# Kernel optimization log

Hardware: AMD Instinct MI355X
Metric: run time of the kernel (lower is better)

## Reference

```python
import jax, jax.numpy as jnp
import numpy as np

FS = 4096.0
TRAIN_KERNEL = 4
TRAIN_STRIDE = 0.25
BATCH = 1024
NPERSEG = 4096          # fftlength * fs
NOVERLAP = NPERSEG // 2 # default overlap
FL, FH = 20.0, 500.0


def _welch(data):
    """Faithful port of _torch_welch with average='mean' (which is a SUM over segments
    in the original code), off by the same constant factor as the original."""
    N, nsample = data.shape
    nstride = NPERSEG - NOVERLAP
    nseg = int(np.ceil((nsample - NPERSEG) / nstride)) + 1
    # frame indices [nseg, nperseg] (static numpy -> cheap gather)
    idx = np.arange(nseg)[:, None] * nstride + np.arange(NPERSEG)[None, :]
    frames = data[:, idx]                                   # [N, nseg, nperseg]
    n = np.arange(NPERSEG)
    window = (0.5 - 0.5 * np.cos(2.0 * np.pi * n / NPERSEG)).astype(np.float32) * 2.0  # periodic hann * 2
    fd = jnp.fft.rfft(frames * window, axis=-1)             # [N, nseg, nfreq]
    power = jnp.real(fd) ** 2 + jnp.imag(fd) ** 2
    psd = jnp.sum(power, axis=1)                            # original 'mean' branch uses sum
    T = nsample * FS
    return psd / T                                          # [N, nfreq]


def setup_inputs() -> dict:
    key = jax.random.key(0)
    k1, k2 = jax.random.split(key)
    T = int(TRAIN_KERNEL * FS)  # 16384
    pred = jax.random.normal(k1, (BATCH, T), dtype=jnp.float32)
    target = jax.random.normal(k2, (BATCH, T), dtype=jnp.float32)
    return {"pred": pred, "target": target}


def reference(pred, target):
    res = target - pred
    s = int(TRAIN_STRIDE * FS)                     # 1024 samples per stride
    shape_x = int(TRAIN_KERNEL / TRAIN_STRIDE)     # 16
    # cross[i] = res[:, i*s:(i+1)*s].flatten() -> reshape/transpose, no loop
    def to_cross(x):
        return x[:, : shape_x * s].reshape(BATCH, shape_x, s).transpose(1, 0, 2).reshape(shape_x, BATCH * s)
    cross_res = to_cross(res)
    cross_target = to_cross(target)

    psd_res = _welch(cross_res)                    # [shape_x, nfreq]
    psd_target = _welch(cross_target)

    nfreq = NPERSEG // 2 + 1
    freq = np.linspace(0.0, FS / 2.0, nfreq)
    mask = jnp.asarray((FL < freq) & (freq < FH))
    dfreq = float(freq[1] - freq[0])
    scale = FH - FL

    psd_res = jnp.where(mask, psd_res, 0.0)
    psd_ratio = psd_res / psd_target
    loss = jnp.sum(psd_ratio, axis=1) * dfreq / scale  # [shape_x]
    return jnp.mean(loss[-8:]) * loss.shape[0]
```

## Files before the change

kernel.cpp:

```cpp
#include <hip/hip_runtime.h>

#define NSEG 511
#define NROWS 8
#define ROW0 8
#define K0 21
#define KEND 500
#define NFREQ 479
#define ACC_STRIDE 512
#define ACC_ELEMS (2 * NROWS * ACC_STRIDE)
#define NREP 8
#define SPB 4
#define NGROUPS 128
#define NBLOCKS (2 * NROWS * NGROUPS)

__device__ __forceinline__ int sw(int i) { return i ^ (((i >> 5) & 7) << 2); }
__device__ __forceinline__ int ms(int m) { return m ^ ((m >> 6) & 7); }

__device__ __forceinline__ float2 cmul(float2 a, float2 b) {
    return make_float2(fmaf(a.x, b.x, -a.y * b.y), fmaf(a.x, b.y, a.y * b.x));
}
__device__ __forceinline__ float2 cadd(float2 a, float2 b) { return make_float2(a.x + b.x, a.y + b.y); }
__device__ __forceinline__ float2 csub(float2 a, float2 b) { return make_float2(a.x - b.x, a.y - b.y); }

__device__ __forceinline__ void dft8(float2& x0, float2& x1, float2& x2, float2& x3,
                                     float2& x4, float2& x5, float2& x6, float2& x7) {
    const float C45 = 0.70710678118654752440f;
    float2 t0 = cadd(x0, x4), u0 = csub(x0, x4);
    float2 t1 = cadd(x1, x5), u1 = csub(x1, x5);
    float2 t2 = cadd(x2, x6), u2 = csub(x2, x6);
    float2 t3 = cadd(x3, x7), u3 = csub(x3, x7);
    float2 s0 = cadd(t0, t2), d0 = csub(t0, t2);
    float2 s1 = cadd(t1, t3), d1 = csub(t1, t3);
    float2 v1 = make_float2(C45 * (u1.x + u1.y), C45 * (u1.y - u1.x));
    float2 v2 = make_float2(u2.y, -u2.x);
    float2 v3 = make_float2(C45 * (u3.y - u3.x), -C45 * (u3.x + u3.y));
    float2 s2 = cadd(u0, v2), d2 = csub(u0, v2);
    float2 s3 = cadd(v1, v3), d3 = csub(v1, v3);
    float2 mid1 = make_float2(d1.y, -d1.x);
    float2 mid3 = make_float2(d3.y, -d3.x);
    x0 = cadd(s0, s1); x4 = csub(s0, s1);
    x2 = cadd(d0, mid1); x6 = csub(d0, mid1);
    x1 = cadd(s2, s3); x5 = csub(s2, s3);
    x3 = cadd(d2, mid3); x7 = csub(d2, mid3);
}

__device__ __forceinline__ void twiddle8cs(float2& x1, float2& x2, float2& x3, float2& x4,
                                           float2& x5, float2& x6, float2& x7,
                                           float c, float s) {
    float2 w1 = make_float2(c, s);
    float2 w2 = cmul(w1, w1);
    float2 w3 = cmul(w2, w1);
    float2 w4 = cmul(w2, w2);
    float2 w5 = cmul(w4, w1);
    float2 w6 = cmul(w3, w3);
    float2 w7 = cmul(w4, w3);
    x1 = cmul(x1, w1); x2 = cmul(x2, w2); x3 = cmul(x3, w3);
    x4 = cmul(x4, w4); x5 = cmul(x5, w5); x6 = cmul(x6, w6);
    x7 = cmul(x7, w7);
}

__global__ __launch_bounds__(256)
void psd_kernel(const float* __restrict__ pred,
                const float* __restrict__ target,
                float* __restrict__ acc) {
    __shared__ float2 buf[2048];
    __shared__ float2 nat[1024];

    const int bid = blockIdx.x;
    const int grp = bid % NGROUPS;
    const int row = (bid / NGROUPS) % NROWS + ROW0;
    const int sig = bid / (NGROUPS * NROWS);
    const int tid = threadIdx.x;
    const int seg0 = grp * SPB;
    const int ns = (seg0 + SPB <= NSEG) ? SPB : (NSEG - seg0);
    float* accR = acc + (bid & (NREP - 1)) * ACC_ELEMS;

    const float2* t2p = (const float2*)target;
    const float2* p2p = (const float2*)pred;

    const int base = 2 * seg0 * 8192 + row * 512 + tid;
#define LOADRAW(X, IDX)                                                      \
    {                                                                        \
        int _i = (IDX);                                                      \
        float2 v = t2p[_i];                                                  \
        if (sig == 0) { float2 p = p2p[_i]; v.x -= p.x; v.y -= p.y; }        \
        X = v;                                                               \
    }
    float2 r0, r1, r2, r3, r4, r5, r6, r7;
    LOADRAW(r0, base)
    LOADRAW(r1, base + 256)
    LOADRAW(r2, base + 8192)
    LOADRAW(r3, base + 8448)
    LOADRAW(r4, base + 16384)
    LOADRAW(r5, base + 16640)
    LOADRAW(r6, base + 24576)
    LOADRAW(r7, base + 24832)

    const float WA = 3.06796157577128245e-3f;
    const float CD = 0.99999882344642529f;
    const float SD = 1.53398018628476550e-3f;
    const float H  = 0.70710678118654752440f;
    float sa, ca;
    __sincosf((float)tid * WA, &sa, &ca);
    float2 wv0, wv1, wv2, wv3, wv4, wv5, wv6, wv7;
#define MKW(W, CE, SE) { float cr = (CE), sr = (SE);                         \
        W = make_float2(1.0f - cr, 1.0f - (cr * CD - sr * SD)); }
    MKW(wv0, ca, sa)
    MKW(wv1, H * (ca - sa), H * (sa + ca))
    MKW(wv2, -sa, ca)
    MKW(wv3, -H * (ca + sa), H * (ca - sa))
    MKW(wv4, -ca, -sa)
    MKW(wv5, H * (sa - ca), -H * (sa + ca))
    MKW(wv6, sa, -ca)
    MKW(wv7, H * (ca + sa), H * (sa - ca))
#undef MKW
    float sb, cb;
    __sincosf((float)(tid & 31) * -2.45436926061702596e-2f, &sb, &cb);
    float cc, ss;
    {
        const float TC1 = 0.98078528040323044913f, TS1 = -0.19509032201612826785f;
        const float TC2 = 0.92387953251128675613f, TS2 = -0.38268343236508977173f;
        const float TC3 = 0.83146961230254523708f, TS3 = -0.55557023301960222474f;
        int mq = tid & 3;
        cc = (mq & 2) ? ((mq & 1) ? TC3 : TC2) : ((mq & 1) ? TC1 : 1.0f);
        ss = (mq & 2) ? ((mq & 1) ? TS3 : TS2) : ((mq & 1) ? TS1 : 0.0f);
    }
    float sn0, cs0, sn1, cs1;
    __sincosf(-1.53398078788564123e-3f * (float)(K0 + tid), &sn0, &cs0);
    {
        const float CU = 0.98078528040323044913f;
        const float SU = 0.19509032201612826785f;
        cs1 = cs0 * CU + sn0 * SU;
        sn1 = sn0 * CU - cs0 * SU;
    }

    float pw1 = 0.0f, pw2 = 0.0f;
    float4* b4 = (float4*)buf;

    #pragma unroll 1
    for (int s = 0; s < ns; ++s) {
        float2 x0 = make_float2(r0.x * wv0.x, r0.y * wv0.y);
        float2 x1 = make_float2(r1.x * wv1.x, r1.y * wv1.y);
        float2 x2 = make_float2(r2.x * wv2.x, r2.y * wv2.y);
        float2 x3 = make_float2(r3.x * wv3.x, r3.y * wv3.y);
        float2 x4 = make_float2(r4.x * wv4.x, r4.y * wv4.y);
        float2 x5 = make_float2(r5.x * wv5.x, r5.y * wv5.y);
        float2 x6 = make_float2(r6.x * wv6.x, r6.y * wv6.y);
        float2 x7 = make_float2(r7.x * wv7.x, r7.y * wv7.y);

        if (s + 1 < ns) {
            r0 = r4; r1 = r5; r2 = r6; r3 = r7;
            int nb = base + (s + 1) * 16384;
            LOADRAW(r4, nb + 16384)
            LOADRAW(r5, nb + 16640)
            LOADRAW(r6, nb + 24576)
            LOADRAW(r7, nb + 24832)
        }

        dft8(x0, x1, x2, x3, x4, x5, x6, x7);
        twiddle8cs(x1, x2, x3, x4, x5, x6, x7, ca, -sa);
        buf[sw(tid)]        = x0;
        buf[sw(tid + 256)]  = x1;
        buf[sw(tid + 512)]  = x2;
        buf[sw(tid + 768)]  = x3;
        buf[sw(tid + 1024)] = x4;
        buf[sw(tid + 1280)] = x5;
        buf[sw(tid + 1536)] = x6;
        buf[sw(tid + 1792)] = x7;
        __syncthreads();

        {
            const int baseB = (tid & 31) + 256 * (tid >> 5);
            x0 = buf[sw(baseB)];
            x1 = buf[sw(baseB + 32)];
            x2 = buf[sw(baseB + 64)];
            x3 = buf[sw(baseB + 96)];
            x4 = buf[sw(baseB + 128)];
            x5 = buf[sw(baseB + 160)];
            x6 = buf[sw(baseB + 192)];
            x7 = buf[sw(baseB + 224)];
            dft8(x0, x1, x2, x3, x4, x5, x6, x7);
            twiddle8cs(x1, x2, x3, x4, x5, x6, x7, cb, sb);
            buf[sw(baseB)]       = x0;
            buf[sw(baseB + 32)]  = x1;
            buf[sw(baseB + 64)]  = x2;
            buf[sw(baseB + 96)]  = x3;
            buf[sw(baseB + 128)] = x4;
            buf[sw(baseB + 160)] = x5;
            buf[sw(baseB + 192)] = x6;
            buf[sw(baseB + 224)] = x7;
        }
        __syncthreads();

        {
            const int baseC = (tid & 3) + 32 * ((tid >> 2) & 7) + 256 * (tid >> 5);
            x0 = buf[sw(baseC)];
            x1 = buf[sw(baseC + 4)];
            x2 = buf[sw(baseC + 8)];
            x3 = buf[sw(baseC + 12)];
            x4 = buf[sw(baseC + 16)];
            x5 = buf[sw(baseC + 20)];
            x6 = buf[sw(baseC + 24)];
            x7 = buf[sw(baseC + 28)];
            dft8(x0, x1, x2, x3, x4, x5, x6, x7);
            twiddle8cs(x1, x2, x3, x4, x5, x6, x7, cc, ss);
            buf[sw(baseC)]      = x0;
            buf[sw(baseC + 4)]  = x1;
            buf[sw(baseC + 8)]  = x2;
            buf[sw(baseC + 12)] = x3;
            buf[sw(baseC + 16)] = x4;
            buf[sw(baseC + 20)] = x5;
            buf[sw(baseC + 24)] = x6;
            buf[sw(baseC + 28)] = x7;
        }
        __syncthreads();

#define QUAD(N)                                                              \
        {                                                                    \
            int n = (N);                                                     \
            int q4 = sw(4 * n) >> 1;                                         \
            float4 lo = b4[q4], hi = b4[q4 + 1];                             \
            float2 X0 = make_float2((lo.x + hi.x) + (lo.z + hi.z),           \
                                    (lo.y + hi.y) + (lo.w + hi.w));          \
            float D0x = lo.x - hi.x, D0y = lo.y - hi.y;                      \
            float D1x = lo.z - hi.z, D1y = lo.w - hi.w;                      \
            float2 X3 = make_float2(D0x - D1y, D0y + D1x);                   \
            int m = 64 * (n & 7) + 8 * ((n >> 3) & 7) + (n >> 6);            \
            int a = ms(m);                                                   \
            nat[a] = X0;                                                     \
            nat[512 + a] = X3;                                               \
        }
        QUAD(tid)
        QUAD(tid + 256)
#undef QUAD
        __syncthreads();

        {
            int k = K0 + tid;
            float2 zk = nat[ms(k)];
            float2 zn = nat[512 + ms(512 - k)];
            float Ex = 0.5f * (zk.x + zn.x);
            float Ey = 0.5f * (zk.y - zn.y);
            float Ox = 0.5f * (zk.y + zn.y);
            float Oy = -0.5f * (zk.x - zn.x);
            float xr = Ex + Ox * cs0 - Oy * sn0;
            float xi = Ey + Ox * sn0 + Oy * cs0;
            pw1 += xr * xr + xi * xi;
        }
        if (tid < KEND - K0 - 256) {
            int k = K0 + 256 + tid;
            float2 zk = nat[ms(k)];
            float2 zn = nat[512 + ms(512 - k)];
            float Ex = 0.5f * (zk.x + zn.x);
            float Ey = 0.5f * (zk.y - zn.y);
            float Ox = 0.5f * (zk.y + zn.y);
            float Oy = -0.5f * (zk.x - zn.x);
            float xr = Ex + Ox * cs1 - Oy * sn1;
            float xi = Ey + Ox * sn1 + Oy * cs1;
            pw2 += xr * xr + xi * xi;
        }
        __syncthreads();
    }

    {
        int i0 = (sig * NROWS + (row - ROW0)) * ACC_STRIDE;
        atomicAdd(&accR[i0 + tid], pw1);
        if (tid < KEND - K0 - 256) atomicAdd(&accR[i0 + 256 + tid], pw2);
    }
#undef LOADRAW
}

__global__ __launch_bounds__(256)
void reduce_kernel(const float* __restrict__ acc, float* __restrict__ out) {
    __shared__ float sh[256];
    int tid = threadIdx.x;
    float sum = 0.0f;
    for (int n = tid; n < NROWS * NFREQ; n += 256) {
        int r = n / NFREQ, k = n % NFREQ;
        float num = 0.0f, den = 0.0f;
        #pragma unroll
        for (int rep = 0; rep < NREP; ++rep) {
            num += acc[rep * ACC_ELEMS + r * ACC_STRIDE + k];
            den += acc[rep * ACC_ELEMS + (NROWS + r) * ACC_STRIDE + k];
        }
        sum += num / den;
    }
    sh[tid] = sum;
    __syncthreads();
    for (int s = 128; s > 0; s >>= 1) {
        if (tid < s) sh[tid] += sh[tid + s];
        __syncthreads();
    }
    if (tid == 0) out[0] = sh[0] * (1.0f / 240.0f);
}

extern "C" void kernel_launch(void* const* d_in, const int* in_sizes, int n_in,
                              void* d_out, int out_size, void* d_ws, size_t ws_size,
                              hipStream_t stream) {
    const float* pred = (const float*)d_in[0];
    const float* target = (const float*)d_in[1];
    float* acc = (float*)d_ws;

    hipMemsetAsync(acc, 0, NREP * ACC_ELEMS * sizeof(float), stream);
    psd_kernel<<<NBLOCKS, 256, 0, stream>>>(pred, target, acc);
    reduce_kernel<<<1, 256, 0, stream>>>(acc, (float*)d_out);
}
```

Measured before the change: 170.2 us.

## Fuse final radix-4 stage into the power epilogue and drop syncs

The intermediate `nat` shared buffer and its scatter pass are removed. Each thread now reads the needed quads straight from `buf` using precomputed bit-reversed indices and does the final radix-4 butterfly inline during the PSD accumulation. This cuts a full LDS write/read round trip and two barriers per segment. The trailing barrier is now skipped on the last iteration. The barrier between the second and third FFT stages is dropped, which relies on each stage's data staying within one wavefront. Window coefficients are recomputed each iteration behind an asm barrier to cut register pressure, and launch bounds request 6 blocks per CU, trading extra ALU work for occupancy.

```diff
diff --git a/kernel.cpp b/kernel.cpp
--- a/kernel.cpp
+++ b/kernel.cpp
@@ -14,7 +14,7 @@
 #define NBLOCKS (2 * NROWS * NGROUPS)
 
 __device__ __forceinline__ int sw(int i) { return i ^ (((i >> 5) & 7) << 2); }
-__device__ __forceinline__ int ms(int m) { return m ^ ((m >> 6) & 7); }
+__device__ __forceinline__ int revq(int m) { return 64 * (m & 7) + 8 * ((m >> 3) & 7) + (m >> 6); }
 
 __device__ __forceinline__ float2 cmul(float2 a, float2 b) {
     return make_float2(fmaf(a.x, b.x, -a.y * b.y), fmaf(a.x, b.y, a.y * b.x));
@@ -59,12 +59,11 @@
     x7 = cmul(x7, w7);
 }
 
-__global__ __launch_bounds__(256)
+__global__ __launch_bounds__(256, 6)
 void psd_kernel(const float* __restrict__ pred,
                 const float* __restrict__ target,
                 float* __restrict__ acc) {
     __shared__ float2 buf[2048];
-    __shared__ float2 nat[1024];
 
     const int bid = blockIdx.x;
     const int grp = bid % NGROUPS;
@@ -102,18 +101,6 @@
     const float H  = 0.70710678118654752440f;
     float sa, ca;
     __sincosf((float)tid * WA, &sa, &ca);
-    float2 wv0, wv1, wv2, wv3, wv4, wv5, wv6, wv7;
-#define MKW(W, CE, SE) { float cr = (CE), sr = (SE);                         \
-        W = make_float2(1.0f - cr, 1.0f - (cr * CD - sr * SD)); }
-    MKW(wv0, ca, sa)
-    MKW(wv1, H * (ca - sa), H * (sa + ca))
-    MKW(wv2, -sa, ca)
-    MKW(wv3, -H * (ca + sa), H * (ca - sa))
-    MKW(wv4, -ca, -sa)
-    MKW(wv5, H * (sa - ca), -H * (sa + ca))
-    MKW(wv6, sa, -ca)
-    MKW(wv7, H * (ca + sa), H * (sa - ca))
-#undef MKW
     float sb, cb;
     __sincosf((float)(tid & 31) * -2.45436926061702596e-2f, &sb, &cb);
     float cc, ss;
@@ -133,12 +120,34 @@
         cs1 = cs0 * CU + sn0 * SU;
         sn1 = sn0 * CU - cs0 * SU;
     }
+    const int qA1 = sw(4 * revq(K0 + tid)) >> 1;
+    const int qB1 = sw(4 * revq(512 - (K0 + tid))) >> 1;
+    int qA2 = 0, qB2 = 0;
+    if (tid < KEND - K0 - 256) {
+        qA2 = sw(4 * revq(K0 + 256 + tid)) >> 1;
+        qB2 = sw(4 * revq(512 - (K0 + 256 + tid))) >> 1;
+    }
 
     float pw1 = 0.0f, pw2 = 0.0f;
     float4* b4 = (float4*)buf;
 
     #pragma unroll 1
     for (int s = 0; s < ns; ++s) {
+        float cat = ca, sat = sa;
+        asm volatile("" : "+v"(cat), "+v"(sat));
+        float2 wv0, wv1, wv2, wv3, wv4, wv5, wv6, wv7;
+#define MKW(W, CE, SE) { float cr = (CE), sr = (SE);                         \
+        W = make_float2(1.0f - cr, 1.0f - (cr * CD - sr * SD)); }
+        MKW(wv0, cat, sat)
+        MKW(wv1, H * (cat - sat), H * (sat + cat))
+        MKW(wv2, -sat, cat)
+        MKW(wv3, -H * (cat + sat), H * (cat - sat))
+        MKW(wv4, -cat, -sat)
+        MKW(wv5, H * (sat - cat), -H * (sat + cat))
+        MKW(wv6, sat, -cat)
+        MKW(wv7, H * (cat + sat), H * (sat - cat))
+#undef MKW
+
         float2 x0 = make_float2(r0.x * wv0.x, r0.y * wv0.y);
         float2 x1 = make_float2(r1.x * wv1.x, r1.y * wv1.y);
         float2 x2 = make_float2(r2.x * wv2.x, r2.y * wv2.y);
@@ -190,7 +199,6 @@
             buf[sw(baseB + 192)] = x6;
             buf[sw(baseB + 224)] = x7;
         }
-        __syncthreads();
 
         {
             const int baseC = (tid & 3) + 32 * ((tid >> 2) & 7) + 256 * (tid >> 5);
@@ -215,30 +223,14 @@
         }
         __syncthreads();
 
-#define QUAD(N)                                                              \
-        {                                                                    \
-            int n = (N);                                                     \
-            int q4 = sw(4 * n) >> 1;                                         \
-            float4 lo = b4[q4], hi = b4[q4 + 1];                             \
-            float2 X0 = make_float2((lo.x + hi.x) + (lo.z + hi.z),           \
-                                    (lo.y + hi.y) + (lo.w + hi.w));          \
-            float D0x = lo.x - hi.x, D0y = lo.y - hi.y;                      \
-            float D1x = lo.z - hi.z, D1y = lo.w - hi.w;                      \
-            float2 X3 = make_float2(D0x - D1y, D0y + D1x);                   \
-            int m = 64 * (n & 7) + 8 * ((n >> 3) & 7) + (n >> 6);            \
-            int a = ms(m);                                                   \
-            nat[a] = X0;                                                     \
-            nat[512 + a] = X3;                                               \
-        }
-        QUAD(tid)
-        QUAD(tid + 256)
-#undef QUAD
-        __syncthreads();
-
         {
-            int k = K0 + tid;
-            float2 zk = nat[ms(k)];
-            float2 zn = nat[512 + ms(512 - k)];
+            float4 lo = b4[qA1], hi = b4[qA1 + 1];
+            float2 zk = make_float2((lo.x + hi.x) + (lo.z + hi.z),
+                                    (lo.y + hi.y) + (lo.w + hi.w));
+            lo = b4[qB1]; hi = b4[qB1 + 1];
+            float D0x = lo.x - hi.x, D0y = lo.y - hi.y;
+            float D1x = lo.z - hi.z, D1y = lo.w - hi.w;
+            float2 zn = make_float2(D0x - D1y, D0y + D1x);
             float Ex = 0.5f * (zk.x + zn.x);
             float Ey = 0.5f * (zk.y - zn.y);
             float Ox = 0.5f * (zk.y + zn.y);
@@ -248,9 +240,13 @@
             pw1 += xr * xr + xi * xi;
         }
         if (tid < KEND - K0 - 256) {
-            int k = K0 + 256 + tid;
-            float2 zk = nat[ms(k)];
-            float2 zn = nat[512 + ms(512 - k)];
+            float4 lo = b4[qA2], hi = b4[qA2 + 1];
+            float2 zk = make_float2((lo.x + hi.x) + (lo.z + hi.z),
+                                    (lo.y + hi.y) + (lo.w + hi.w));
+            lo = b4[qB2]; hi = b4[qB2 + 1];
+            float D0x = lo.x - hi.x, D0y = lo.y - hi.y;
+            float D1x = lo.z - hi.z, D1y = lo.w - hi.w;
+            float2 zn = make_float2(D0x - D1y, D0y + D1x);
             float Ex = 0.5f * (zk.x + zn.x);
             float Ey = 0.5f * (zk.y - zn.y);
             float Ox = 0.5f * (zk.y + zn.y);
@@ -259,7 +255,7 @@
             float xi = Ey + Ox * sn1 + Oy * cs1;
             pw2 += xr * xr + xi * xi;
         }
-        __syncthreads();
+        if (s + 1 < ns) __syncthreads();
     }
 
     {
```

Measured after the change: 273.1 us. 1.6x slower.
